# Performance work log

Measured on AMD Instinct MI355X. Metric: run time of the kernel, lower is better.

## Reference

```python
import jax, jax.numpy as jnp
import numpy as np

EPS = 1e-5
N_HEAD = 8
N_FREQS = 65
EMB_DIM = 128
E_DIM = 4            # ceil(256 / 65)
V_DIM = EMB_DIM // N_HEAD
CTX = 10


def prelu(x, a):
    return jnp.where(x >= 0, x, a * x)


def ln_last(x, g, b):
    # LayerNormalization4DCF_new: normalize over the fused (freq, chan) last axis
    mu = jnp.mean(x, axis=-1, keepdims=True)
    var = jnp.mean((x - mu) ** 2, axis=-1, keepdims=True)
    return (x - mu) / jnp.sqrt(var + EPS) * g + b


def head_proj(x, W, b, a, g, bt, H, Dh):
    # x: [B, T, F, C] -> [B*H, T, F*Dh], LayerNorm over last dim
    B, T, F, C = x.shape
    y = prelu(jnp.einsum('btfc,oc->btfo', x, W) + b, a)
    y = y.reshape(B, T, F, H, Dh).transpose(0, 3, 1, 2, 4).reshape(B * H, T, F * Dh)
    return ln_last(y, g, bt)


def setup_inputs() -> dict:
    key = jax.random.key(0)
    ks = jax.random.split(key, 8)
    B, T = 4, 500
    d = {}
    d['x'] = jax.random.normal(ks[0], (B, EMB_DIM, N_FREQS, T), dtype=jnp.float32)
    d['merged_context'] = jax.random.normal(ks[1], (B, EMB_DIM, N_FREQS, T), dtype=jnp.float32)
    d['K_buf'] = jnp.zeros((B * N_HEAD, CTX - 1, N_FREQS * E_DIM), dtype=jnp.float32)
    d['V_buf'] = jnp.zeros((B * N_HEAD, CTX - 1, N_FREQS * V_DIM), dtype=jnp.float32)
    d['W_Q'] = jax.random.normal(ks[2], (E_DIM * N_HEAD, EMB_DIM), dtype=jnp.float32) * 0.05
    d['b_Q'] = jnp.zeros((E_DIM * N_HEAD,), dtype=jnp.float32)
    d['a_Q'] = jnp.full((1,), 0.25, dtype=jnp.float32)
    d['g_Q'] = jnp.ones((N_FREQS * E_DIM,), dtype=jnp.float32)
    d['be_Q'] = jnp.zeros((N_FREQS * E_DIM,), dtype=jnp.float32)
    d['W_K'] = jax.random.normal(ks[3], (E_DIM * N_HEAD, EMB_DIM), dtype=jnp.float32) * 0.05
    d['b_K'] = jnp.zeros((E_DIM * N_HEAD,), dtype=jnp.float32)
    d['a_K'] = jnp.full((1,), 0.25, dtype=jnp.float32)
    d['g_K'] = jnp.ones((N_FREQS * E_DIM,), dtype=jnp.float32)
    d['be_K'] = jnp.zeros((N_FREQS * E_DIM,), dtype=jnp.float32)
    d['W_V'] = jax.random.normal(ks[4], (EMB_DIM, EMB_DIM), dtype=jnp.float32) * 0.05
    d['b_V'] = jnp.zeros((EMB_DIM,), dtype=jnp.float32)
    d['a_V'] = jnp.full((1,), 0.25, dtype=jnp.float32)
    d['g_V'] = jnp.ones((N_FREQS * V_DIM,), dtype=jnp.float32)
    d['be_V'] = jnp.zeros((N_FREQS * V_DIM,), dtype=jnp.float32)
    d['W_P'] = jax.random.normal(ks[5], (EMB_DIM, EMB_DIM), dtype=jnp.float32) * 0.05
    d['b_P'] = jnp.zeros((EMB_DIM,), dtype=jnp.float32)
    d['a_P'] = jnp.full((1,), 0.25, dtype=jnp.float32)
    d['g_P'] = jnp.ones((N_FREQS * EMB_DIM,), dtype=jnp.float32)
    d['be_P'] = jnp.zeros((N_FREQS * EMB_DIM,), dtype=jnp.float32)
    return d


def reference(x, merged_context, K_buf, V_buf,
              W_Q, b_Q, a_Q, g_Q, be_Q,
              W_K, b_K, a_K, g_K, be_K,
              W_V, b_V, a_V, g_V, be_V,
              W_P, b_P, a_P, g_P, be_P):
    # x, merged_context: [B, C, F, T] -> [B, T, F, C]
    xp = jnp.transpose(x, (0, 3, 2, 1))
    mc = jnp.transpose(merged_context, (0, 3, 2, 1))
    B, T, F, C = xp.shape
    H = N_HEAD

    Q = head_proj(xp, W_Q, b_Q, a_Q, g_Q, be_Q, H, E_DIM)     # [B*H, T, F*E]
    K = head_proj(mc, W_K, b_K, a_K, g_K, be_K, H, V_DIM * 0 + E_DIM)
    V = head_proj(mc, W_V, b_V, a_V, g_V, be_V, H, V_DIM)     # [B*H, T, F*Vd]

    Kfull = jnp.concatenate([K_buf, K], axis=1)               # [B*H, T+ctx-1, F*E]
    Vfull = jnp.concatenate([V_buf, V], axis=1)               # [B*H, T+ctx-1, F*Vd]
    K_buf_new = Kfull[:, -(CTX - 1):]
    V_buf_new = Vfull[:, -(CTX - 1):]

    # causal sliding windows of length ctx: [B*H, T, ctx, D]
    idx = jnp.arange(T)[:, None] + jnp.arange(CTX)[None, :]
    Kw = Kfull[:, idx, :]
    Vw = Vfull[:, idx, :]

    dqk = F * E_DIM
    scores = jnp.einsum('btd,btcd->btc', Q, Kw) / jnp.sqrt(jnp.float32(dqk))
    p = jax.nn.softmax(scores, axis=-1)                        # [B*H, T, ctx]
    Vo = jnp.einsum('btc,btcd->btd', p, Vw)                    # [B*H, T, F*Vd]

    # reassemble channels: [B*H, T, F*Vd] -> [B, T, F, H*Vd]
    z = Vo.reshape(B, H, T, F, V_DIM).transpose(0, 2, 3, 1, 4).reshape(B, T, F, H * V_DIM)

    y = prelu(jnp.einsum('btfc,oc->btfo', z, W_P) + b_P, a_P)  # [B, T, F, C]
    y = ln_last(y.reshape(B, T, F * C), g_P, be_P).reshape(B, T, F, C)

    out = y + xp
    out = jnp.transpose(out, (0, 3, 2, 1))                     # [B, C, F, T]
    return out, K_buf_new, V_buf_new
```

## Files before the change

kernel.cpp:

```cpp
#include <hip/hip_runtime.h>
#include <math.h>

#define NB   4
#define NT   500
#define NF   65
#define NC   128
#define NH   8
#define NE   4
#define NV   16
#define NCTX 10
#define DQ   260
#define DV   1040
#define DP   8320

#define MQ 0
#define RQ 16000
#define MK 32000
#define RK 48000
#define MV 64000
#define RV 80000

__global__ __launch_bounds__(256, 4) void proj32_k(const float* __restrict__ x,
    const float* __restrict__ W, const float* __restrict__ bias,
    const float* __restrict__ a, float* __restrict__ out,
    float* __restrict__ sS, float* __restrict__ sS2)
{
    __shared__ float Wl[NC * 32];
    int b = blockIdx.x / NF, f = blockIdx.x % NF;
    for (int idx = threadIdx.x; idx < 32 * NC; idx += 256) {
        int o = idx & 31, c = idx >> 5;
        Wl[c * 32 + o] = W[o * NC + c];
    }
    __syncthreads();
    int og = threadIdx.x >> 6;
    int tg = threadIdx.x & 63;
    int t0 = blockIdx.y * 128 + tg * 2;
    int t0c = t0 <= NT - 2 ? t0 : NT - 2;
    const float* xp = x + ((size_t)(b * NC) * NF + f) * NT + t0c;
    const float* wp = Wl + og * 8;
    float2 acc[8];
#pragma unroll
    for (int i = 0; i < 8; i++) acc[i] = make_float2(0.f, 0.f);
#pragma unroll 4
    for (int c = 0; c < NC; c++) {
        float2 xv = *(const float2*)(xp + (size_t)c * (NF * NT));
        const float* wc = wp + c * 32;
        float wv[8];
        *(float4*)(wv)     = *(const float4*)(wc);
        *(float4*)(wv + 4) = *(const float4*)(wc + 4);
#pragma unroll
        for (int i = 0; i < 8; i++) {
            acc[i].x += xv.x * wv[i];
            acc[i].y += xv.y * wv[i];
        }
    }
    if (t0 > NT - 2) return;
    float av = a[0];
#pragma unroll
    for (int i = 0; i < 8; i++) {
        int o = og * 8 + i;
        float vx = acc[i].x + bias[o], vy = acc[i].y + bias[o];
        vx = vx >= 0.f ? vx : av * vx;
        vy = vy >= 0.f ? vy : av * vy;
        acc[i].x = vx; acc[i].y = vy;
        int h = o >> 2, e = o & 3;
        *(float2*)(out + ((size_t)(b * NH + h) * DQ + f * NE + e) * NT + t0) = acc[i];
    }
#pragma unroll
    for (int hh = 0; hh < 2; hh++) {
        int h = og * 2 + hh;
        float sx = 0.f, sy = 0.f, qx = 0.f, qy = 0.f;
#pragma unroll
        for (int e = 0; e < 4; e++) {
            float2 v = acc[hh * 4 + e];
            sx += v.x; sy += v.y; qx += v.x * v.x; qy += v.y * v.y;
        }
        int base = (b * NH + h) * NT + t0;
        atomicAdd(&sS[base], sx);      atomicAdd(&sS[base + 1], sy);
        atomicAdd(&sS2[base], qx);     atomicAdd(&sS2[base + 1], qy);
    }
}

__global__ __launch_bounds__(256, 4) void projV_k(const float* __restrict__ x,
    const float* __restrict__ W, const float* __restrict__ bias,
    const float* __restrict__ a, float* __restrict__ out,
    float* __restrict__ sS, float* __restrict__ sS2)
{
    __shared__ float Wl[NC * 64];
    int b = blockIdx.x / NF, f = blockIdx.x % NF;
    int o0 = blockIdx.z * 64;
    for (int idx = threadIdx.x; idx < 64 * NC; idx += 256) {
        int o = idx & 63, c = idx >> 6;
        Wl[c * 64 + o] = W[(o0 + o) * NC + c];
    }
    __syncthreads();
    int og = threadIdx.x >> 6;
    int tg = threadIdx.x & 63;
    int t0 = blockIdx.y * 128 + tg * 2;
    int t0c = t0 <= NT - 2 ? t0 : NT - 2;
    const float* xp = x + ((size_t)(b * NC) * NF + f) * NT + t0c;
    const float* wp = Wl + og * 16;
    float2 acc[16];
#pragma unroll
    for (int i = 0; i < 16; i++) acc[i] = make_float2(0.f, 0.f);
#pragma unroll 2
    for (int c = 0; c < NC; c++) {
        float2 xv = *(const float2*)(xp + (size_t)c * (NF * NT));
        const float* wc = wp + c * 64;
        float wv[16];
        *(float4*)(wv)      = *(const float4*)(wc);
        *(float4*)(wv + 4)  = *(const float4*)(wc + 4);
        *(float4*)(wv + 8)  = *(const float4*)(wc + 8);
        *(float4*)(wv + 12) = *(const float4*)(wc + 12);
#pragma unroll
        for (int i = 0; i < 16; i++) {
            acc[i].x += xv.x * wv[i];
            acc[i].y += xv.y * wv[i];
        }
    }
    if (t0 > NT - 2) return;
    float av = a[0];
    int h = (o0 >> 4) + og;
    float sx = 0.f, sy = 0.f, qx = 0.f, qy = 0.f;
#pragma unroll
    for (int i = 0; i < 16; i++) {
        int o = o0 + og * 16 + i;
        float vx = acc[i].x + bias[o], vy = acc[i].y + bias[o];
        vx = vx >= 0.f ? vx : av * vx;
        vy = vy >= 0.f ? vy : av * vy;
        *(float2*)(out + ((size_t)(b * NH + h) * DV + f * NV + i) * NT + t0) = make_float2(vx, vy);
        sx += vx; sy += vy; qx += vx * vx; qy += vy * vy;
    }
    int base = (b * NH + h) * NT + t0;
    atomicAdd(&sS[base], sx);      atomicAdd(&sS[base + 1], sy);
    atomicAdd(&sS2[base], qx);     atomicAdd(&sS2[base + 1], qy);
}

__global__ __launch_bounds__(256, 4) void projP_k(const float* __restrict__ VoT,
    const float* __restrict__ W, const float* __restrict__ bias,
    const float* __restrict__ a, float* __restrict__ yraw,
    float* __restrict__ sP, float* __restrict__ s2P)
{
    __shared__ float Wl[NC * 64];
    int b = blockIdx.x / NF, f = blockIdx.x % NF;
    int o0 = blockIdx.z * 64;
    for (int idx = threadIdx.x; idx < 64 * NC; idx += 256) {
        int o = idx & 63, c = idx >> 6;
        Wl[c * 64 + o] = W[(o0 + o) * NC + c];
    }
    __syncthreads();
    int og = threadIdx.x >> 6;
    int tg = threadIdx.x & 63;
    int t0 = blockIdx.y * 128 + tg * 2;
    int t0c = t0 <= NT - 2 ? t0 : NT - 2;
    const float* zp = VoT + ((size_t)(b * NH) * DV + f * NV) * NT + t0c;
    const float* wp = Wl + og * 16;
    float2 acc[16];
#pragma unroll
    for (int i = 0; i < 16; i++) acc[i] = make_float2(0.f, 0.f);
    for (int hc = 0; hc < NH; hc++) {
        const float* zh = zp + (size_t)hc * DV * NT;
        const float* wh = wp + hc * 16 * 64;
#pragma unroll
        for (int v = 0; v < NV; v++) {
            float2 xv = *(const float2*)(zh + (size_t)v * NT);
            const float* wc = wh + v * 64;
            float wv[16];
            *(float4*)(wv)      = *(const float4*)(wc);
            *(float4*)(wv + 4)  = *(const float4*)(wc + 4);
            *(float4*)(wv + 8)  = *(const float4*)(wc + 8);
            *(float4*)(wv + 12) = *(const float4*)(wc + 12);
#pragma unroll
            for (int i = 0; i < 16; i++) {
                acc[i].x += xv.x * wv[i];
                acc[i].y += xv.y * wv[i];
            }
        }
    }
    if (t0 > NT - 2) return;
    float av = a[0];
    float sx = 0.f, sy = 0.f, qx = 0.f, qy = 0.f;
#pragma unroll
    for (int i = 0; i < 16; i++) {
        int o = o0 + og * 16 + i;
        float vx = acc[i].x + bias[o], vy = acc[i].y + bias[o];
        vx = vx >= 0.f ? vx : av * vx;
        vy = vy >= 0.f ? vy : av * vy;
        *(float2*)(yraw + ((size_t)(b * NC + o) * NF + f) * NT + t0) = make_float2(vx, vy);
        sx += vx; sy += vy; qx += vx * vx; qy += vy * vy;
    }
    int base = b * NT + t0;
    atomicAdd(&sP[base], sx);      atomicAdd(&sP[base + 1], sy);
    atomicAdd(&s2P[base], qx);     atomicAdd(&s2P[base + 1], qy);
}

__global__ __launch_bounds__(256) void finqkv_k(const float* __restrict__ stats,
    float* __restrict__ murs)
{
    int i = blockIdx.x * 256 + threadIdx.x;
    if (i >= 48000) return;
    int seg = i / 16000, j = i % 16000;
    float S = stats[seg * 32000 + j], S2 = stats[seg * 32000 + 16000 + j];
    float D = (seg < 2) ? 260.f : 1040.f;
    float mu = S / D;
    float var = S2 / D - mu * mu;
    murs[seg * 32000 + j] = mu;
    murs[seg * 32000 + 16000 + j] = rsqrtf(var + 1e-5f);
}

__global__ __launch_bounds__(256) void finp_k(const float* __restrict__ sP,
    const float* __restrict__ s2P, float* __restrict__ muP, float* __restrict__ rsP)
{
    int i = blockIdx.x * 256 + threadIdx.x;
    if (i >= NB * NT) return;
    float inv = 1.0f / (float)DP;
    float mu = sP[i] * inv;
    float var = s2P[i] * inv - mu * mu;
    muP[i] = mu;
    rsP[i] = rsqrtf(var + 1e-5f);
}

__global__ void copybuf_k(const float* __restrict__ Kt, const float* __restrict__ Vt,
    const float* __restrict__ murs,
    const float* __restrict__ g_K, const float* __restrict__ be_K,
    const float* __restrict__ g_V, const float* __restrict__ be_V,
    float* __restrict__ outK, float* __restrict__ outV)
{
    int i = blockIdx.x * 256 + threadIdx.x;
    const int NK = 32 * 9 * DQ;
    const int NVb = 32 * 9 * DV;
    if (i < NK) {
        int bh = i / (9 * DQ); int r = i % (9 * DQ); int j = r / DQ; int d = r % DQ;
        int tt = 491 + j;
        float v = Kt[(size_t)(bh * DQ + d) * NT + tt];
        float mu = murs[MK + bh * NT + tt], rs = murs[RK + bh * NT + tt];
        outK[i] = (v - mu) * rs * g_K[d] + be_K[d];
    } else if (i < NK + NVb) {
        int i2 = i - NK;
        int bh = i2 / (9 * DV); int r = i2 % (9 * DV); int j = r / DV; int d = r % DV;
        int tt = 491 + j;
        float v = Vt[(size_t)(bh * DV + d) * NT + tt];
        float mu = murs[MV + bh * NT + tt], rs = murs[RV + bh * NT + tt];
        outV[i2] = (v - mu) * rs * g_V[d] + be_V[d];
    }
}

__global__ __launch_bounds__(128) void scores_s1_k(const float* __restrict__ Qt,
    const float* __restrict__ Kt, const float* __restrict__ Kbuf,
    const float* __restrict__ murs,
    const float* __restrict__ g_Q, const float* __restrict__ be_Q,
    const float* __restrict__ g_K, const float* __restrict__ be_K,
    float* __restrict__ spart)
{
    int bh = blockIdx.x;
    int t = blockIdx.y * 128 + threadIdx.x;
    if (t >= NT) return;
    int z = blockIdx.z;
    int d0 = z * 13;
    float rsq = murs[RQ + bh * NT + t];
    float mq = -murs[MQ + bh * NT + t] * rsq;
    float s[NCTX];
    if (t >= NCTX - 1) {
        float rkc[NCTX], mkc[NCTX];
#pragma unroll
        for (int c = 0; c < NCTX; c++) {
            int tk = t - (NCTX - 1) + c;
            rkc[c] = murs[RK + bh * NT + tk];
            mkc[c] = -murs[MK + bh * NT + tk] * rkc[c];
        }
        float A[NCTX], SG = 0.f, SB = 0.f;
#pragma unroll
        for (int c = 0; c < NCTX; c++) A[c] = 0.f;
        const float* qp = Qt + ((size_t)bh * DQ + d0) * NT + t;
        const float* kp = Kt + ((size_t)bh * DQ + d0) * NT + (t - (NCTX - 1));
#pragma unroll 4
        for (int d = 0; d < 13; d++) {
            float gq = g_Q[d0 + d], bq = be_Q[d0 + d];
            float gk = g_K[d0 + d], bk = be_K[d0 + d];
            float qln = (qp[(size_t)d * NT] * rsq + mq) * gq + bq;
            float qg = qln * gk;
            SG += qg; SB += qln * bk;
            const float* kr = kp + (size_t)d * NT;
#pragma unroll
            for (int c = 0; c < NCTX; c++) A[c] += qg * kr[c];
        }
#pragma unroll
        for (int c = 0; c < NCTX; c++) s[c] = rkc[c] * A[c] + mkc[c] * SG + SB;
    } else {
#pragma unroll
        for (int c = 0; c < NCTX; c++) s[c] = 0.f;
        for (int d = 0; d < 13; d++) {
            float gq = g_Q[d0 + d], bq = be_Q[d0 + d];
            float gk = g_K[d0 + d], bk = be_K[d0 + d];
            float qln = (Qt[((size_t)bh * DQ + d0 + d) * NT + t] * rsq + mq) * gq + bq;
#pragma unroll
            for (int c = 0; c < NCTX; c++) {
                int tc = t + c;
                float kv;
                if (tc < NCTX - 1) {
                    kv = Kbuf[((size_t)bh * (NCTX - 1) + tc) * DQ + d0 + d];
                } else {
                    int tk = tc - (NCTX - 1);
                    float rk = murs[RK + bh * NT + tk];
                    float mk = murs[MK + bh * NT + tk];
                    kv = (Kt[((size_t)bh * DQ + d0 + d) * NT + tk] - mk) * rk * gk + bk;
                }
                s[c] += qln * kv;
            }
        }
    }
#pragma unroll
    for (int c = 0; c < NCTX; c++)
        spart[(size_t)((z * 32 + bh) * NCTX + c) * NT + t] = s[c];
}

__global__ __launch_bounds__(128) void softmax_k(const float* __restrict__ spart,
    float* __restrict__ p)
{
    int bh = blockIdx.x;
    int t = blockIdx.y * 128 + threadIdx.x;
    if (t >= NT) return;
    float s[NCTX];
#pragma unroll
    for (int c = 0; c < NCTX; c++) s[c] = 0.f;
    for (int z = 0; z < 20; z++) {
#pragma unroll
        for (int c = 0; c < NCTX; c++)
            s[c] += spart[(size_t)((z * 32 + bh) * NCTX + c) * NT + t];
    }
    const float sc = 0.06201736729460423f;
    float m = -1e30f;
#pragma unroll
    for (int c = 0; c < NCTX; c++) { s[c] *= sc; m = fmaxf(m, s[c]); }
    float den = 0.f;
#pragma unroll
    for (int c = 0; c < NCTX; c++) { s[c] = __expf(s[c] - m); den += s[c]; }
    float iden = 1.0f / den;
#pragma unroll
    for (int c = 0; c < NCTX; c++) p[(size_t)(bh * NCTX + c) * NT + t] = s[c] * iden;
}

__global__ __launch_bounds__(128) void vo_k(const float* __restrict__ p,
    const float* __restrict__ Vt, const float* __restrict__ Vbuf,
    const float* __restrict__ murs,
    const float* __restrict__ g_V, const float* __restrict__ be_V,
    float* __restrict__ VoT)
{
    int bh = blockIdx.x;
    int t = blockIdx.y * 128 + threadIdx.x;
    if (t >= NT) return;
    int d0 = blockIdx.z * 16;
    float pc[NCTX];
#pragma unroll
    for (int c = 0; c < NCTX; c++) pc[c] = p[(size_t)(bh * NCTX + c) * NT + t];
    if (t >= NCTX - 1) {
        float prs[NCTX], Cm = 0.f, Cp = 0.f;
#pragma unroll
        for (int c = 0; c < NCTX; c++) {
            int tv = t - (NCTX - 1) + c;
            float rs = murs[RV + bh * NT + tv];
            prs[c] = pc[c] * rs;
            Cm += pc[c] * (-murs[MV + bh * NT + tv] * rs);
            Cp += pc[c];
        }
        const float* vp = Vt + ((size_t)bh * DV + d0) * NT + (t - (NCTX - 1));
        float* op = VoT + ((size_t)bh * DV + d0) * NT + t;
#pragma unroll 4
        for (int d = 0; d < 16; d++) {
            float gv = g_V[d0 + d], bv = be_V[d0 + d];
            const float* vr = vp + (size_t)d * NT;
            float A = 0.f;
#pragma unroll
            for (int c = 0; c < NCTX; c++) A += prs[c] * vr[c];
            op[(size_t)d * NT] = gv * (A + Cm) + bv * Cp;
        }
    } else {
        for (int d = 0; d < 16; d++) {
            float gv = g_V[d0 + d], bv = be_V[d0 + d];
            float acc = 0.f;
#pragma unroll
            for (int c = 0; c < NCTX; c++) {
                int tc = t + c;
                float v;
                if (tc < NCTX - 1) {
                    v = Vbuf[((size_t)bh * (NCTX - 1) + tc) * DV + d0 + d];
                } else {
                    int tv = tc - (NCTX - 1);
                    float rs = murs[RV + bh * NT + tv];
                    float mu = murs[MV + bh * NT + tv];
                    v = (Vt[((size_t)bh * DV + d0 + d) * NT + tv] - mu) * rs * gv + bv;
                }
                acc += pc[c] * v;
            }
            VoT[((size_t)bh * DV + d0 + d) * NT + t] = acc;
        }
    }
}

__global__ __launch_bounds__(256) void lnp_apply(const float* __restrict__ yraw,
    const float* __restrict__ x, const float* __restrict__ g, const float* __restrict__ be,
    const float* __restrict__ muA, const float* __restrict__ rstdA, float* __restrict__ out)
{
    int bo = blockIdx.x; int b = bo >> 7, o = bo & 127;
    int t = blockIdx.y * 256 + threadIdx.x;
    if (t >= NT) return;
    float mu = muA[b * NT + t], rstd = rstdA[b * NT + t];
    for (int f = 0; f < NF; f++) {
        size_t idx = (size_t)((b * NC + o) * NF + f) * NT + t;
        int i = f * NC + o;
        float v = yraw[idx];
        out[idx] = (v - mu) * rstd * g[i] + be[i] + x[idx];
    }
}

extern "C" void kernel_launch(void* const* d_in, const int* in_sizes, int n_in,
                              void* d_out, int out_size, void* d_ws, size_t ws_size,
                              hipStream_t stream) {
    const float* x    = (const float*)d_in[0];
    const float* mc   = (const float*)d_in[1];
    const float* Kbuf = (const float*)d_in[2];
    const float* Vbuf = (const float*)d_in[3];
    const float* W_Q  = (const float*)d_in[4];
    const float* b_Q  = (const float*)d_in[5];
    const float* a_Q  = (const float*)d_in[6];
    const float* g_Q  = (const float*)d_in[7];
    const float* be_Q = (const float*)d_in[8];
    const float* W_K  = (const float*)d_in[9];
    const float* b_K  = (const float*)d_in[10];
    const float* a_K  = (const float*)d_in[11];
    const float* g_K  = (const float*)d_in[12];
    const float* be_K = (const float*)d_in[13];
    const float* W_V  = (const float*)d_in[14];
    const float* b_V  = (const float*)d_in[15];
    const float* a_V  = (const float*)d_in[16];
    const float* g_V  = (const float*)d_in[17];
    const float* be_V = (const float*)d_in[18];
    const float* W_P  = (const float*)d_in[19];
    const float* b_P  = (const float*)d_in[20];
    const float* a_P  = (const float*)d_in[21];
    const float* g_P  = (const float*)d_in[22];
    const float* be_P = (const float*)d_in[23];

    float* out  = (float*)d_out;
    float* outK = out + (size_t)NB * NC * NF * NT;
    float* outV = outK + 32 * 9 * DQ;

    float* stats = out;
    float* murs  = out + 96000;

    float* ws = (float*)d_ws;
    float* Qt   = ws;
    float* Kt   = Qt + (size_t)32 * DQ * NT;
    float* Vt   = Kt + (size_t)32 * DQ * NT;
    float* VoT  = Vt + (size_t)32 * DV * NT;
    float* pbuf = VoT + (size_t)32 * DV * NT;
    float* sP   = pbuf + (size_t)32 * NCTX * NT;
    float* s2P  = sP + NB * NT;
    float* muP  = s2P + NB * NT;
    float* rsP  = muP + NB * NT;
    float* yraw  = Vt;
    float* spart = VoT;

    dim3 blk(256);
    dim3 blk128(128);
    const int TCH = (NT + 255) / 256;
    const int TCH4 = (NT + 127) / 128;

    hipMemsetAsync(stats, 0, 96000 * sizeof(float), stream);
    hipMemsetAsync(sP, 0, 2 * NB * NT * sizeof(float), stream);

    proj32_k<<<dim3(NB * NF, 4), blk, 0, stream>>>(x,  W_Q, b_Q, a_Q, Qt,
                                                   stats + 0,     stats + 16000);
    proj32_k<<<dim3(NB * NF, 4), blk, 0, stream>>>(mc, W_K, b_K, a_K, Kt,
                                                   stats + 32000, stats + 48000);
    projV_k <<<dim3(NB * NF, 4, 2), blk, 0, stream>>>(mc, W_V, b_V, a_V, Vt,
                                                      stats + 64000, stats + 80000);

    finqkv_k<<<dim3(188), blk, 0, stream>>>(stats, murs);

    int nbuf = 32 * 9 * DQ + 32 * 9 * DV;
    copybuf_k<<<dim3((nbuf + 255) / 256), blk, 0, stream>>>(Kt, Vt, murs,
                                                            g_K, be_K, g_V, be_V, outK, outV);

    scores_s1_k<<<dim3(32, TCH4, 20), blk128, 0, stream>>>(Qt, Kt, Kbuf, murs,
                                                           g_Q, be_Q, g_K, be_K, spart);
    softmax_k  <<<dim3(32, TCH4), blk128, 0, stream>>>(spart, pbuf);
    vo_k       <<<dim3(32, TCH4, 65), blk128, 0, stream>>>(pbuf, Vt, Vbuf, murs,
                                                           g_V, be_V, VoT);

    projP_k<<<dim3(NB * NF, 4, 2), blk, 0, stream>>>(VoT, W_P, b_P, a_P, yraw, sP, s2P);

    finp_k<<<dim3((NB * NT + 255) / 256), blk, 0, stream>>>(sP, s2P, muP, rsP);

    lnp_apply<<<dim3(NB * NC, TCH), blk, 0, stream>>>(yraw, x, g_P, be_P, muP, rsP, out);
}
```

Before: 695.2 us.

## Split reduction dimension across two thread groups in projection kernels

The Q/K, V and output projection kernels now launch 512 threads per block. The two halves each accumulate over half of the input channels (or heads for the output projection), and the partial sums are combined through shared memory reused from the weight tile. This doubles the threads in flight per block to hide global load latency in these memory-bound loops. In exchange it adds two barriers plus a shared-memory reduction, and launch_bounds(512,4) may force register pressure or spills.

New measurement: 697.2 us. About the same (+0.3%).

```diff
diff --git a/kernel.cpp b/kernel.cpp
--- a/kernel.cpp
+++ b/kernel.cpp
@@ -20,30 +20,33 @@
 #define MV 64000
 #define RV 80000
 
-__global__ __launch_bounds__(256, 4) void proj32_k(const float* __restrict__ x,
+__global__ __launch_bounds__(512, 4) void proj32_k(const float* __restrict__ x,
     const float* __restrict__ W, const float* __restrict__ bias,
     const float* __restrict__ a, float* __restrict__ out,
     float* __restrict__ sS, float* __restrict__ sS2)
 {
-    __shared__ float Wl[NC * 32];
+    __shared__ float Wl[4352];
     int b = blockIdx.x / NF, f = blockIdx.x % NF;
-    for (int idx = threadIdx.x; idx < 32 * NC; idx += 256) {
+    for (int idx = threadIdx.x; idx < 32 * NC; idx += 512) {
         int o = idx & 31, c = idx >> 5;
         Wl[c * 32 + o] = W[o * NC + c];
     }
     __syncthreads();
     int og = threadIdx.x >> 6;
+    int cg = og >> 2;
+    int ow = og & 3;
     int tg = threadIdx.x & 63;
     int t0 = blockIdx.y * 128 + tg * 2;
     int t0c = t0 <= NT - 2 ? t0 : NT - 2;
-    const float* xp = x + ((size_t)(b * NC) * NF + f) * NT + t0c;
-    const float* wp = Wl + og * 8;
+    const float* xp = x + ((size_t)(b * NC + cg * 64) * NF + f) * NT + t0c;
+    const float* wp = Wl + cg * 64 * 32 + ow * 8;
+    const size_t xs = (size_t)NF * NT;
     float2 acc[8];
 #pragma unroll
     for (int i = 0; i < 8; i++) acc[i] = make_float2(0.f, 0.f);
 #pragma unroll 4
-    for (int c = 0; c < NC; c++) {
-        float2 xv = *(const float2*)(xp + (size_t)c * (NF * NT));
+    for (int c = 0; c < 64; c++) {
+        float2 xv = *(const float2*)(xp + (size_t)c * xs);
         const float* wc = wp + c * 32;
         float wv[8];
         *(float4*)(wv)     = *(const float4*)(wc);
@@ -54,11 +57,24 @@
             acc[i].y += xv.y * wv[i];
         }
     }
+    __syncthreads();
+    if (cg == 1) {
+        float* rp = Wl + (threadIdx.x & 255) * 17;
+#pragma unroll
+        for (int i = 0; i < 8; i++) { rp[i * 2] = acc[i].x; rp[i * 2 + 1] = acc[i].y; }
+    }
+    __syncthreads();
+    if (cg == 1) return;
+    {
+        const float* rp = Wl + threadIdx.x * 17;
+#pragma unroll
+        for (int i = 0; i < 8; i++) { acc[i].x += rp[i * 2]; acc[i].y += rp[i * 2 + 1]; }
+    }
     if (t0 > NT - 2) return;
     float av = a[0];
 #pragma unroll
     for (int i = 0; i < 8; i++) {
-        int o = og * 8 + i;
+        int o = ow * 8 + i;
         float vx = acc[i].x + bias[o], vy = acc[i].y + bias[o];
         vx = vx >= 0.f ? vx : av * vx;
         vy = vy >= 0.f ? vy : av * vy;
@@ -68,7 +84,7 @@
     }
 #pragma unroll
     for (int hh = 0; hh < 2; hh++) {
-        int h = og * 2 + hh;
+        int h = ow * 2 + hh;
         float sx = 0.f, sy = 0.f, qx = 0.f, qy = 0.f;
 #pragma unroll
         for (int e = 0; e < 4; e++) {
@@ -81,31 +97,34 @@
     }
 }
 
-__global__ __launch_bounds__(256, 4) void projV_k(const float* __restrict__ x,
+__global__ __launch_bounds__(512, 4) void projV_k(const float* __restrict__ x,
     const float* __restrict__ W, const float* __restrict__ bias,
     const float* __restrict__ a, float* __restrict__ out,
     float* __restrict__ sS, float* __restrict__ sS2)
 {
-    __shared__ float Wl[NC * 64];
+    __shared__ float Wl[8448];
     int b = blockIdx.x / NF, f = blockIdx.x % NF;
     int o0 = blockIdx.z * 64;
-    for (int idx = threadIdx.x; idx < 64 * NC; idx += 256) {
+    for (int idx = threadIdx.x; idx < 64 * NC; idx += 512) {
         int o = idx & 63, c = idx >> 6;
         Wl[c * 64 + o] = W[(o0 + o) * NC + c];
     }
     __syncthreads();
     int og = threadIdx.x >> 6;
+    int cg = og >> 2;
+    int ow = og & 3;
     int tg = threadIdx.x & 63;
     int t0 = blockIdx.y * 128 + tg * 2;
     int t0c = t0 <= NT - 2 ? t0 : NT - 2;
-    const float* xp = x + ((size_t)(b * NC) * NF + f) * NT + t0c;
-    const float* wp = Wl + og * 16;
+    const float* xp = x + ((size_t)(b * NC + cg * 64) * NF + f) * NT + t0c;
+    const float* wp = Wl + cg * 64 * 64 + ow * 16;
+    const size_t xs = (size_t)NF * NT;
     float2 acc[16];
 #pragma unroll
     for (int i = 0; i < 16; i++) acc[i] = make_float2(0.f, 0.f);
 #pragma unroll 2
-    for (int c = 0; c < NC; c++) {
-        float2 xv = *(const float2*)(xp + (size_t)c * (NF * NT));
+    for (int c = 0; c < 64; c++) {
+        float2 xv = *(const float2*)(xp + (size_t)c * xs);
         const float* wc = wp + c * 64;
         float wv[16];
         *(float4*)(wv)      = *(const float4*)(wc);
@@ -118,13 +137,26 @@
             acc[i].y += xv.y * wv[i];
         }
     }
+    __syncthreads();
+    if (cg == 1) {
+        float* rp = Wl + (threadIdx.x & 255) * 33;
+#pragma unroll
+        for (int i = 0; i < 16; i++) { rp[i * 2] = acc[i].x; rp[i * 2 + 1] = acc[i].y; }
+    }
+    __syncthreads();
+    if (cg == 1) return;
+    {
+        const float* rp = Wl + threadIdx.x * 33;
+#pragma unroll
+        for (int i = 0; i < 16; i++) { acc[i].x += rp[i * 2]; acc[i].y += rp[i * 2 + 1]; }
+    }
     if (t0 > NT - 2) return;
     float av = a[0];
-    int h = (o0 >> 4) + og;
+    int h = (o0 >> 4) + ow;
     float sx = 0.f, sy = 0.f, qx = 0.f, qy = 0.f;
 #pragma unroll
     for (int i = 0; i < 16; i++) {
-        int o = o0 + og * 16 + i;
+        int o = o0 + ow * 16 + i;
         float vx = acc[i].x + bias[o], vy = acc[i].y + bias[o];
         vx = vx >= 0.f ? vx : av * vx;
         vy = vy >= 0.f ? vy : av * vy;
@@ -136,29 +168,31 @@
     atomicAdd(&sS2[base], qx);     atomicAdd(&sS2[base + 1], qy);
 }
 
-__global__ __launch_bounds__(256, 4) void projP_k(const float* __restrict__ VoT,
+__global__ __launch_bounds__(512, 4) void projP_k(const float* __restrict__ VoT,
     const float* __restrict__ W, const float* __restrict__ bias,
     const float* __restrict__ a, float* __restrict__ yraw,
     float* __restrict__ sP, float* __restrict__ s2P)
 {
-    __shared__ float Wl[NC * 64];
+    __shared__ float Wl[8448];
     int b = blockIdx.x / NF, f = blockIdx.x % NF;
     int o0 = blockIdx.z * 64;
-    for (int idx = threadIdx.x; idx < 64 * NC; idx += 256) {
+    for (int idx = threadIdx.x; idx < 64 * NC; idx += 512) {
         int o = idx & 63, c = idx >> 6;
         Wl[c * 64 + o] = W[(o0 + o) * NC + c];
     }
     __syncthreads();
     int og = threadIdx.x >> 6;
+    int cg = og >> 2;
+    int ow = og & 3;
     int tg = threadIdx.x & 63;
     int t0 = blockIdx.y * 128 + tg * 2;
     int t0c = t0 <= NT - 2 ? t0 : NT - 2;
     const float* zp = VoT + ((size_t)(b * NH) * DV + f * NV) * NT + t0c;
-    const float* wp = Wl + og * 16;
+    const float* wp = Wl + ow * 16;
     float2 acc[16];
 #pragma unroll
     for (int i = 0; i < 16; i++) acc[i] = make_float2(0.f, 0.f);
-    for (int hc = 0; hc < NH; hc++) {
+    for (int hc = cg * 4; hc < cg * 4 + 4; hc++) {
         const float* zh = zp + (size_t)hc * DV * NT;
         const float* wh = wp + hc * 16 * 64;
 #pragma unroll
@@ -177,12 +211,25 @@
             }
         }
     }
+    __syncthreads();
+    if (cg == 1) {
+        float* rp = Wl + (threadIdx.x & 255) * 33;
+#pragma unroll
+        for (int i = 0; i < 16; i++) { rp[i * 2] = acc[i].x; rp[i * 2 + 1] = acc[i].y; }
+    }
+    __syncthreads();
+    if (cg == 1) return;
+    {
+        const float* rp = Wl + threadIdx.x * 33;
+#pragma unroll
+        for (int i = 0; i < 16; i++) { acc[i].x += rp[i * 2]; acc[i].y += rp[i * 2 + 1]; }
+    }
     if (t0 > NT - 2) return;
     float av = a[0];
     float sx = 0.f, sy = 0.f, qx = 0.f, qy = 0.f;
 #pragma unroll
     for (int i = 0; i < 16; i++) {
-        int o = o0 + og * 16 + i;
+        int o = o0 + ow * 16 + i;
         float vx = acc[i].x + bias[o], vy = acc[i].y + bias[o];
         vx = vx >= 0.f ? vx : av * vx;
         vy = vy >= 0.f ? vy : av * vy;
@@ -463,18 +510,19 @@
 
     dim3 blk(256);
     dim3 blk128(128);
+    dim3 blk512(512);
     const int TCH = (NT + 255) / 256;
     const int TCH4 = (NT + 127) / 128;
 
     hipMemsetAsync(stats, 0, 96000 * sizeof(float), stream);
     hipMemsetAsync(sP, 0, 2 * NB * NT * sizeof(float), stream);
 
-    proj32_k<<<dim3(NB * NF, 4), blk, 0, stream>>>(x,  W_Q, b_Q, a_Q, Qt,
-                                                   stats + 0,     stats + 16000);
-    proj32_k<<<dim3(NB * NF, 4), blk, 0, stream>>>(mc, W_K, b_K, a_K, Kt,
-                                                   stats + 32000, stats + 48000);
-    projV_k <<<dim3(NB * NF, 4, 2), blk, 0, stream>>>(mc, W_V, b_V, a_V, Vt,
-                                                      stats + 64000, stats + 80000);
+    proj32_k<<<dim3(NB * NF, 4), blk512, 0, stream>>>(x,  W_Q, b_Q, a_Q, Qt,
+                                                      stats + 0,     stats + 16000);
+    proj32_k<<<dim3(NB * NF, 4), blk512, 0, stream>>>(mc, W_K, b_K, a_K, Kt,
+                                                      stats + 32000, stats + 48000);
+    projV_k <<<dim3(NB * NF, 4, 2), blk512, 0, stream>>>(mc, W_V, b_V, a_V, Vt,
+                                                         stats + 64000, stats + 80000);
 
     finqkv_k<<<dim3(188), blk, 0, stream>>>(stats, murs);
 
@@ -488,7 +536,7 @@
     vo_k       <<<dim3(32, TCH4, 65), blk128, 0, stream>>>(pbuf, Vt, Vbuf, murs,
                                                            g_V, be_V, VoT);
 
-    projP_k<<<dim3(NB * NF, 4, 2), blk, 0, stream>>>(VoT, W_P, b_P, a_P, yraw, sP, s2P);
+    projP_k<<<dim3(NB * NF, 4, 2), blk512, 0, stream>>>(VoT, W_P, b_P, a_P, yraw, sP, s2P);
 
     finp_k<<<dim3((NB * NT + 255) / 256), blk, 0, stream>>>(sP, s2P, muP, rsP);
 
```

## Pre-transpose weights once and read them via scalar loads in projection kernels

Applied to the files above, without the earlier changes.

A single transW_k kernel now transposes all four weight matrices into a workspace up front. The projection kernels drop their per-block shared-memory weight staging and __syncthreads, and read weights through a wave-uniform index (readfirstlane), so the loads can go through the scalar path. Q and K projections are merged into one launch, and V/P use 8 outputs per thread with twice as many blocks, with launch bounds raised for occupancy. The trade-off is that each x/VoT element is now re-read by more blocks, because output channels are split more finely.

Result: slower. 717.5 us (+3.2%).

```diff
diff --git a/kernel.cpp b/kernel.cpp
--- a/kernel.cpp
+++ b/kernel.cpp
@@ -20,46 +20,75 @@
 #define MV 64000
 #define RV 80000
 
-__global__ __launch_bounds__(256, 4) void proj32_k(const float* __restrict__ x,
-    const float* __restrict__ W, const float* __restrict__ bias,
-    const float* __restrict__ a, float* __restrict__ out,
-    float* __restrict__ sS, float* __restrict__ sS2)
-{
-    __shared__ float Wl[NC * 32];
+#define WTQ 0
+#define WTK 4096
+#define WTV 8192
+#define WTP 24576
+
+__global__ __launch_bounds__(256) void transW_k(const float* __restrict__ WQ,
+    const float* __restrict__ WK, const float* __restrict__ WV,
+    const float* __restrict__ WP, float* __restrict__ Wt)
+{
+    int i = blockIdx.x * 256 + threadIdx.x;
+    if (i < 4096) {
+        int c = i >> 5, o = i & 31;
+        Wt[WTQ + c * 32 + o] = WQ[o * 128 + c];
+    } else if (i < 8192) {
+        int j = i - 4096; int c = j >> 5, o = j & 31;
+        Wt[WTK + c * 32 + o] = WK[o * 128 + c];
+    } else if (i < 24576) {
+        int j = i - 8192; int c = j >> 7, o = j & 127;
+        Wt[WTV + c * 128 + o] = WV[o * 128 + c];
+    } else if (i < 40960) {
+        int j = i - 24576; int c = j >> 7, o = j & 127;
+        Wt[WTP + c * 128 + o] = WP[o * 128 + c];
+    }
+}
+
+__global__ __launch_bounds__(256, 6) void projQK_k(const float* __restrict__ x,
+    const float* __restrict__ mc, const float* __restrict__ Wt,
+    const float* __restrict__ bQ, const float* __restrict__ bK,
+    const float* __restrict__ aQ, const float* __restrict__ aK,
+    float* __restrict__ Qt, float* __restrict__ Kt,
+    float* __restrict__ stats)
+{
+    int z = blockIdx.z;
+    const float* xin  = z ? mc : x;
+    const float* wt   = Wt + (z ? WTK : WTQ);
+    const float* bias = z ? bK : bQ;
+    const float* ap   = z ? aK : aQ;
+    float* out = z ? Kt : Qt;
+    float* sS  = stats + z * 32000;
+    float* sS2 = sS + 16000;
     int b = blockIdx.x / NF, f = blockIdx.x % NF;
-    for (int idx = threadIdx.x; idx < 32 * NC; idx += 256) {
-        int o = idx & 31, c = idx >> 5;
-        Wl[c * 32 + o] = W[o * NC + c];
-    }
-    __syncthreads();
-    int og = threadIdx.x >> 6;
-    int tg = threadIdx.x & 63;
-    int t0 = blockIdx.y * 128 + tg * 2;
-    int t0c = t0 <= NT - 2 ? t0 : NT - 2;
-    const float* xp = x + ((size_t)(b * NC) * NF + f) * NT + t0c;
-    const float* wp = Wl + og * 8;
+    int w = threadIdx.x >> 6, l = threadIdx.x & 63;
+    int o0 = __builtin_amdgcn_readfirstlane(w * 8);
+    int t0 = blockIdx.y * 128 + l * 2;
+    bool act = (t0 < NT - 1);
+    int t0c = act ? t0 : NT - 2;
+    const size_t xs = (size_t)NF * NT;
+    const float* xp = xin + (size_t)(b * NC) * xs + (size_t)f * NT + t0c;
     float2 acc[8];
 #pragma unroll
     for (int i = 0; i < 8; i++) acc[i] = make_float2(0.f, 0.f);
 #pragma unroll 4
     for (int c = 0; c < NC; c++) {
-        float2 xv = *(const float2*)(xp + (size_t)c * (NF * NT));
-        const float* wc = wp + c * 32;
-        float wv[8];
-        *(float4*)(wv)     = *(const float4*)(wc);
-        *(float4*)(wv + 4) = *(const float4*)(wc + 4);
+        float2 xv = *(const float2*)(xp + (size_t)c * xs);
+        const float* wr = wt + c * 32 + o0;
 #pragma unroll
         for (int i = 0; i < 8; i++) {
-            acc[i].x += xv.x * wv[i];
-            acc[i].y += xv.y * wv[i];
-        }
-    }
-    if (t0 > NT - 2) return;
-    float av = a[0];
+            float wv = wr[i];
+            acc[i].x += wv * xv.x;
+            acc[i].y += wv * xv.y;
+        }
+    }
+    if (!act) return;
+    float av = ap[0];
 #pragma unroll
     for (int i = 0; i < 8; i++) {
-        int o = og * 8 + i;
-        float vx = acc[i].x + bias[o], vy = acc[i].y + bias[o];
+        int o = o0 + i;
+        float bo = bias[o];
+        float vx = acc[i].x + bo, vy = acc[i].y + bo;
         vx = vx >= 0.f ? vx : av * vx;
         vy = vy >= 0.f ? vy : av * vy;
         acc[i].x = vx; acc[i].y = vy;
@@ -68,11 +97,11 @@
     }
 #pragma unroll
     for (int hh = 0; hh < 2; hh++) {
-        int h = og * 2 + hh;
+        int h = (o0 >> 2) + hh;
         float sx = 0.f, sy = 0.f, qx = 0.f, qy = 0.f;
 #pragma unroll
-        for (int e = 0; e < 4; e++) {
-            float2 v = acc[hh * 4 + e];
+        for (int i = 0; i < 4; i++) {
+            float2 v = acc[hh * 4 + i];
             sx += v.x; sy += v.y; qx += v.x * v.x; qy += v.y * v.y;
         }
         int base = (b * NH + h) * NT + t0;
@@ -81,54 +110,47 @@
     }
 }
 
-__global__ __launch_bounds__(256, 4) void projV_k(const float* __restrict__ x,
-    const float* __restrict__ W, const float* __restrict__ bias,
+__global__ __launch_bounds__(256, 6) void projV_k(const float* __restrict__ xin,
+    const float* __restrict__ Wt, const float* __restrict__ bias,
     const float* __restrict__ a, float* __restrict__ out,
     float* __restrict__ sS, float* __restrict__ sS2)
 {
-    __shared__ float Wl[NC * 64];
     int b = blockIdx.x / NF, f = blockIdx.x % NF;
-    int o0 = blockIdx.z * 64;
-    for (int idx = threadIdx.x; idx < 64 * NC; idx += 256) {
-        int o = idx & 63, c = idx >> 6;
-        Wl[c * 64 + o] = W[(o0 + o) * NC + c];
-    }
-    __syncthreads();
-    int og = threadIdx.x >> 6;
-    int tg = threadIdx.x & 63;
-    int t0 = blockIdx.y * 128 + tg * 2;
-    int t0c = t0 <= NT - 2 ? t0 : NT - 2;
-    const float* xp = x + ((size_t)(b * NC) * NF + f) * NT + t0c;
-    const float* wp = Wl + og * 16;
-    float2 acc[16];
-#pragma unroll
-    for (int i = 0; i < 16; i++) acc[i] = make_float2(0.f, 0.f);
-#pragma unroll 2
+    int oc = blockIdx.z * 32;
+    int w = threadIdx.x >> 6, l = threadIdx.x & 63;
+    int o0 = __builtin_amdgcn_readfirstlane(oc + w * 8);
+    int t0 = blockIdx.y * 128 + l * 2;
+    bool act = (t0 < NT - 1);
+    int t0c = act ? t0 : NT - 2;
+    const size_t xs = (size_t)NF * NT;
+    const float* xp = xin + (size_t)(b * NC) * xs + (size_t)f * NT + t0c;
+    const float* wt = Wt + o0;
+    float2 acc[8];
+#pragma unroll
+    for (int i = 0; i < 8; i++) acc[i] = make_float2(0.f, 0.f);
+#pragma unroll 4
     for (int c = 0; c < NC; c++) {
-        float2 xv = *(const float2*)(xp + (size_t)c * (NF * NT));
-        const float* wc = wp + c * 64;
-        float wv[16];
-        *(float4*)(wv)      = *(const float4*)(wc);
-        *(float4*)(wv + 4)  = *(const float4*)(wc + 4);
-        *(float4*)(wv + 8)  = *(const float4*)(wc + 8);
-        *(float4*)(wv + 12) = *(const float4*)(wc + 12);
-#pragma unroll
-        for (int i = 0; i < 16; i++) {
-            acc[i].x += xv.x * wv[i];
-            acc[i].y += xv.y * wv[i];
-        }
-    }
-    if (t0 > NT - 2) return;
+        float2 xv = *(const float2*)(xp + (size_t)c * xs);
+        const float* wr = wt + c * 128;
+#pragma unroll
+        for (int i = 0; i < 8; i++) {
+            float wv = wr[i];
+            acc[i].x += wv * xv.x;
+            acc[i].y += wv * xv.y;
+        }
+    }
+    if (!act) return;
     float av = a[0];
-    int h = (o0 >> 4) + og;
+    int h = o0 >> 4;
     float sx = 0.f, sy = 0.f, qx = 0.f, qy = 0.f;
 #pragma unroll
-    for (int i = 0; i < 16; i++) {
-        int o = o0 + og * 16 + i;
-        float vx = acc[i].x + bias[o], vy = acc[i].y + bias[o];
+    for (int i = 0; i < 8; i++) {
+        int o = o0 + i;
+        float bo = bias[o];
+        float vx = acc[i].x + bo, vy = acc[i].y + bo;
         vx = vx >= 0.f ? vx : av * vx;
         vy = vy >= 0.f ? vy : av * vy;
-        *(float2*)(out + ((size_t)(b * NH + h) * DV + f * NV + i) * NT + t0) = make_float2(vx, vy);
+        *(float2*)(out + ((size_t)(b * NH + h) * DV + f * NV + (o & 15)) * NT + t0) = make_float2(vx, vy);
         sx += vx; sy += vy; qx += vx * vx; qy += vy * vy;
     }
     int base = (b * NH + h) * NT + t0;
@@ -136,54 +158,46 @@
     atomicAdd(&sS2[base], qx);     atomicAdd(&sS2[base + 1], qy);
 }
 
-__global__ __launch_bounds__(256, 4) void projP_k(const float* __restrict__ VoT,
-    const float* __restrict__ W, const float* __restrict__ bias,
+__global__ __launch_bounds__(256, 6) void projP_k(const float* __restrict__ VoT,
+    const float* __restrict__ Wt, const float* __restrict__ bias,
     const float* __restrict__ a, float* __restrict__ yraw,
     float* __restrict__ sP, float* __restrict__ s2P)
 {
-    __shared__ float Wl[NC * 64];
     int b = blockIdx.x / NF, f = blockIdx.x % NF;
-    int o0 = blockIdx.z * 64;
-    for (int idx = threadIdx.x; idx < 64 * NC; idx += 256) {
-        int o = idx & 63, c = idx >> 6;
-        Wl[c * 64 + o] = W[(o0 + o) * NC + c];
-    }
-    __syncthreads();
-    int og = threadIdx.x >> 6;
-    int tg = threadIdx.x & 63;
-    int t0 = blockIdx.y * 128 + tg * 2;
-    int t0c = t0 <= NT - 2 ? t0 : NT - 2;
-    const float* zp = VoT + ((size_t)(b * NH) * DV + f * NV) * NT + t0c;
-    const float* wp = Wl + og * 16;
-    float2 acc[16];
-#pragma unroll
-    for (int i = 0; i < 16; i++) acc[i] = make_float2(0.f, 0.f);
+    int oc = blockIdx.z * 32;
+    int w = threadIdx.x >> 6, l = threadIdx.x & 63;
+    int o0 = __builtin_amdgcn_readfirstlane(oc + w * 8);
+    int t0 = blockIdx.y * 128 + l * 2;
+    bool act = (t0 < NT - 1);
+    int t0c = act ? t0 : NT - 2;
+    const float* zb = VoT + ((size_t)(b * NH) * DV + f * NV) * NT + t0c;
+    const float* wt = Wt + o0;
+    float2 acc[8];
+#pragma unroll
+    for (int i = 0; i < 8; i++) acc[i] = make_float2(0.f, 0.f);
     for (int hc = 0; hc < NH; hc++) {
-        const float* zh = zp + (size_t)hc * DV * NT;
-        const float* wh = wp + hc * 16 * 64;
-#pragma unroll
+        const float* zh = zb + (size_t)hc * DV * NT;
+        const float* wh = wt + hc * 16 * 128;
+#pragma unroll 4
         for (int v = 0; v < NV; v++) {
             float2 xv = *(const float2*)(zh + (size_t)v * NT);
-            const float* wc = wh + v * 64;
-            float wv[16];
-            *(float4*)(wv)      = *(const float4*)(wc);
-            *(float4*)(wv + 4)  = *(const float4*)(wc + 4);
-            *(float4*)(wv + 8)  = *(const float4*)(wc + 8);
-            *(float4*)(wv + 12) = *(const float4*)(wc + 12);
-#pragma unroll
-            for (int i = 0; i < 16; i++) {
-                acc[i].x += xv.x * wv[i];
-                acc[i].y += xv.y * wv[i];
+            const float* wr = wh + v * 128;
+#pragma unroll
+            for (int i = 0; i < 8; i++) {
+                float wv = wr[i];
+                acc[i].x += wv * xv.x;
+                acc[i].y += wv * xv.y;
             }
         }
     }
-    if (t0 > NT - 2) return;
+    if (!act) return;
     float av = a[0];
     float sx = 0.f, sy = 0.f, qx = 0.f, qy = 0.f;
 #pragma unroll
-    for (int i = 0; i < 16; i++) {
-        int o = o0 + og * 16 + i;
-        float vx = acc[i].x + bias[o], vy = acc[i].y + bias[o];
+    for (int i = 0; i < 8; i++) {
+        int o = o0 + i;
+        float bo = bias[o];
+        float vx = acc[i].x + bo, vy = acc[i].y + bo;
         vx = vx >= 0.f ? vx : av * vx;
         vy = vy >= 0.f ? vy : av * vy;
         *(float2*)(yraw + ((size_t)(b * NC + o) * NF + f) * NT + t0) = make_float2(vx, vy);
@@ -458,6 +472,7 @@
     float* s2P  = sP + NB * NT;
     float* muP  = s2P + NB * NT;
     float* rsP  = muP + NB * NT;
+    float* Wt   = rsP + NB * NT;
     float* yraw  = Vt;
     float* spart = VoT;
 
@@ -469,11 +484,11 @@
     hipMemsetAsync(stats, 0, 96000 * sizeof(float), stream);
     hipMemsetAsync(sP, 0, 2 * NB * NT * sizeof(float), stream);
 
-    proj32_k<<<dim3(NB * NF, 4), blk, 0, stream>>>(x,  W_Q, b_Q, a_Q, Qt,
-                                                   stats + 0,     stats + 16000);
-    proj32_k<<<dim3(NB * NF, 4), blk, 0, stream>>>(mc, W_K, b_K, a_K, Kt,
-                                                   stats + 32000, stats + 48000);
-    projV_k <<<dim3(NB * NF, 4, 2), blk, 0, stream>>>(mc, W_V, b_V, a_V, Vt,
+    transW_k<<<dim3(160), blk, 0, stream>>>(W_Q, W_K, W_V, W_P, Wt);
+
+    projQK_k<<<dim3(NB * NF, 4, 2), blk, 0, stream>>>(x, mc, Wt, b_Q, b_K, a_Q, a_K,
+                                                      Qt, Kt, stats);
+    projV_k <<<dim3(NB * NF, 4, 4), blk, 0, stream>>>(mc, Wt + WTV, b_V, a_V, Vt,
                                                       stats + 64000, stats + 80000);
 
     finqkv_k<<<dim3(188), blk, 0, stream>>>(stats, murs);
@@ -488,7 +503,7 @@
     vo_k       <<<dim3(32, TCH4, 65), blk128, 0, stream>>>(pbuf, Vt, Vbuf, murs,
                                                            g_V, be_V, VoT);
 
-    projP_k<<<dim3(NB * NF, 4, 2), blk, 0, stream>>>(VoT, W_P, b_P, a_P, yraw, sP, s2P);
+    projP_k<<<dim3(NB * NF, 4, 4), blk, 0, stream>>>(VoT, Wt + WTP, b_P, a_P, yraw, sP, s2P);
 
     finp_k<<<dim3((NB * NT + 255) / 256), blk, 0, stream>>>(sP, s2P, muP, rsP);
 
```
